# Performance work log

Measured on AMD Instinct MI355X. Metric: run time of the kernel, lower is better.

## Reference

```python
import jax, jax.numpy as jnp
import numpy as np

B, C, D, H, W = 4, 256, 32, 32, 32
K = 1024  # codebook size


def setup_inputs() -> dict:
    key = jax.random.key(0)
    k1, k2 = jax.random.split(key)
    z = jax.random.normal(k1, (B, C, D, H, W), dtype=jnp.float32)
    # torch init: uniform(-1/K, 1/K)
    emb_weight = jax.random.uniform(k2, (K, C), dtype=jnp.float32,
                                    minval=-1.0 / K, maxval=1.0 / K)
    return {"z": z, "emb_weight": emb_weight}


def reference(z, emb_weight):
    beta = 0.25
    emb_dim = emb_weight.shape[1]
    # [B, C, D, H, W] -> [B, D, H, W, C]
    zc = jnp.transpose(z, (0, 2, 3, 4, 1))
    z_flat = zc.reshape(-1, emb_dim)  # [N, C]
    # squared euclidean distances [N, K]
    d = (jnp.sum(z_flat ** 2, axis=1, keepdims=True)
         + jnp.sum(emb_weight ** 2, axis=1)
         - 2.0 * jnp.matmul(z_flat, emb_weight.T))
    idx = jnp.argmin(d, axis=1)  # [N]
    z_q = emb_weight[idx].reshape(zc.shape)  # [B, D, H, W, C]
    sg = jax.lax.stop_gradient
    loss = jnp.mean((sg(z_q) - zc) ** 2) + beta * jnp.mean((z_q - sg(zc)) ** 2)
    # straight-through estimator
    z_q = zc + sg(z_q - zc)
    # back to [B, C, D, H, W]
    z_q = jnp.transpose(z_q, (0, 4, 1, 2, 3))
    return z_q, loss, idx
```

## Files before the change

### kernel.cpp

```cpp
#include <hip/hip_runtime.h>

#define SPATIAL 32768
#define BATCH   4
#define CH      256
#define KCODES  1024
#define NPTS    (BATCH*SPATIAL)
#define ZQ_SIZE (BATCH*CH*SPATIAL)

#define WS_LOSS  0
#define WS_CNT   8
#define WS_ENORM 16
#define WS_EH    4112
#define WS_EL    (WS_EH + KCODES*CH*2)
#define WS_FLAGS (WS_EL + KCODES*CH*2)

#define MARG 1.5e-4f

typedef _Float16 f16x8 __attribute__((ext_vector_type(8)));
typedef float    f32x4 __attribute__((ext_vector_type(4)));

__global__ __launch_bounds__(256) void vq_prep(const float* __restrict__ emb,
                                               _Float16* __restrict__ eh,
                                               _Float16* __restrict__ el) {
  int i = blockIdx.x * 256 + threadIdx.x;
  float es = emb[i] * 1024.0f;
  _Float16 h = (_Float16)es;
  eh[i] = h;
  el[i] = (_Float16)(es - (float)h);
}

__global__ __launch_bounds__(256) void vq_enorm(const float* __restrict__ emb,
                                                float* __restrict__ enorm) {
  int k = blockIdx.x * 256 + threadIdx.x;
  const float* e = emb + (size_t)k * CH;
  double s = 0.0;
#pragma unroll 8
  for (int c = 0; c < CH; ++c) s = fma((double)e[c], (double)e[c], s);
  enorm[k] = (float)s;
}

__global__ __launch_bounds__(256) void vq_main(
    const float* __restrict__ z, const _Float16* __restrict__ eh_g,
    const _Float16* __restrict__ el_g, const float* __restrict__ enorm,
    float* __restrict__ out_idx, double* __restrict__ loss_acc,
    int* __restrict__ flag_cnt, int* __restrict__ flags) {
  __shared__ _Float16 zh[64][264];
  __shared__ _Float16 zl[64][264];
  __shared__ double   znp[4][64];
  __shared__ float    znb[64];
  __shared__ float rm1s[4][64];
  __shared__ float rm2s[4][64];
  __shared__ int   ri1s[4][64];

  int tid = threadIdx.x;
  int w = tid >> 6;
  int lane = tid & 63;
  int n0 = blockIdx.x * 64;
  int b = n0 / SPATIAL, s0 = n0 % SPATIAL;
  const float* zb = z + (size_t)b * CH * SPATIAL + s0;

  {
    int pt = lane, crow = w;
    const float* zcol = zb + pt;
    double zacc = 0.0;
#pragma unroll
    for (int oct = 0; oct < 8; ++oct) {
      int c0 = crow * 64 + oct * 8;
      f16x8 h8, l8;
#pragma unroll
      for (int i = 0; i < 8; ++i) {
        float v = zcol[(size_t)(c0 + i) * SPATIAL];
        zacc = fma((double)v, (double)v, zacc);
        _Float16 h = (_Float16)v;
        h8[i] = h;
        l8[i] = (_Float16)(v - (float)h);
      }
      *(f16x8*)&zh[pt][c0] = h8;
      *(f16x8*)&zl[pt][c0] = l8;
    }
    znp[crow][pt] = zacc;
  }
  __syncthreads();
  if (tid < 64)
    znb[tid] = (float)(znp[0][tid] + znp[1][tid] + znp[2][tid] + znp[3][tid]);
  __syncthreads();

  int hq = lane >> 4;
  int lr = lane & 15;

  float en_reg[16];
#pragma unroll
  for (int kt = 0; kt < 8; ++kt) {
    en_reg[kt * 2]     = enorm[kt * 128 + w * 32 + lr];
    en_reg[kt * 2 + 1] = enorm[kt * 128 + w * 32 + lr + 16];
  }
  float znr[16];
#pragma unroll
  for (int m = 0; m < 4; ++m)
#pragma unroll
    for (int r = 0; r < 4; ++r)
      znr[m * 4 + r] = znb[m * 16 + hq * 4 + r];

  float rm1[16], rm2[16];
  int   ri1[16];
#pragma unroll
  for (int q = 0; q < 16; ++q) { rm1[q] = 1e30f; rm2[q] = 1e30f; ri1[q] = 0; }

  for (int kt = 0; kt < 8; ++kt) {
    int k0 = kt * 128;
    f32x4 acc[4][2];
#pragma unroll
    for (int m = 0; m < 4; ++m)
#pragma unroll
      for (int n = 0; n < 2; ++n) acc[m][n] = (f32x4){0.f, 0.f, 0.f, 0.f};

#pragma unroll 2
    for (int cc = 0; cc < 8; ++cc) {
      int ca = cc * 32 + hq * 8;
      f16x8 ah[4], al[4], bh[2], bl[2];
#pragma unroll
      for (int m = 0; m < 4; ++m) {
        ah[m] = *(const f16x8*)&zh[m * 16 + lr][ca];
        al[m] = *(const f16x8*)&zl[m * 16 + lr][ca];
      }
#pragma unroll
      for (int n = 0; n < 2; ++n) {
        int code = k0 + w * 32 + n * 16 + lr;
        bh[n] = *(const f16x8*)&eh_g[(size_t)code * CH + ca];
        bl[n] = *(const f16x8*)&el_g[(size_t)code * CH + ca];
      }
#pragma unroll
      for (int m = 0; m < 4; ++m)
#pragma unroll
        for (int n = 0; n < 2; ++n) {
          acc[m][n] = __builtin_amdgcn_mfma_f32_16x16x32_f16(ah[m], bh[n], acc[m][n], 0, 0, 0);
          acc[m][n] = __builtin_amdgcn_mfma_f32_16x16x32_f16(al[m], bh[n], acc[m][n], 0, 0, 0);
          acc[m][n] = __builtin_amdgcn_mfma_f32_16x16x32_f16(ah[m], bl[n], acc[m][n], 0, 0, 0);
        }
    }

    float enA = en_reg[kt * 2], enB = en_reg[kt * 2 + 1];
    int c0i = k0 + w * 32 + lr;
#pragma unroll
    for (int m = 0; m < 4; ++m) {
#pragma unroll
      for (int r = 0; r < 4; ++r) {
        int q = m * 4 + r;
        float zn = znr[q];
        float p0 = (zn + enA) - acc[m][0][r] * 0x1p-9f;
        float p1 = (zn + enB) - acc[m][1][r] * 0x1p-9f;
        if (p0 < rm1[q]) { rm2[q] = rm1[q]; rm1[q] = p0; ri1[q] = c0i; }
        else             { rm2[q] = fminf(rm2[q], p0); }
        if (p1 < rm1[q]) { rm2[q] = rm1[q]; rm1[q] = p1; ri1[q] = c0i + 16; }
        else             { rm2[q] = fminf(rm2[q], p1); }
      }
    }
  }

#pragma unroll
  for (int m = 0; m < 4; ++m) {
#pragma unroll
    for (int r = 0; r < 4; ++r) {
      int q = m * 4 + r;
      float m1 = rm1[q], m2 = rm2[q];
      int i1 = ri1[q];
#pragma unroll
      for (int msk = 1; msk <= 8; msk <<= 1) {
        float om1 = __shfl_xor(m1, msk);
        float om2 = __shfl_xor(m2, msk);
        int   oi1 = __shfl_xor(i1, msk);
        if (om1 < m1 || (om1 == m1 && oi1 < i1)) {
          m2 = fminf(m1, om2); m1 = om1; i1 = oi1;
        } else {
          m2 = fminf(m2, om1);
        }
      }
      if (lr == 0) {
        int pt = m * 16 + hq * 4 + r;
        rm1s[w][pt] = m1; rm2s[w][pt] = m2; ri1s[w][pt] = i1;
      }
    }
  }
  __syncthreads();

  double dv = 0.0;
  if (tid < 64) {
    float m1 = rm1s[0][tid], m2 = rm2s[0][tid];
    int i1 = ri1s[0][tid];
#pragma unroll
    for (int pq = 1; pq < 4; ++pq) {
      float a1 = rm1s[pq][tid], a2 = rm2s[pq][tid];
      int ai = ri1s[pq][tid];
      if (a1 < m1 || (a1 == m1 && ai < i1)) {
        m2 = fminf(m1, a2); m1 = a1; i1 = ai;
      } else {
        m2 = fminf(m2, a1);
      }
    }
    int n = n0 + tid;
    out_idx[n] = (float)i1;
    if (m2 - m1 <= MARG) {
      int p = atomicAdd(flag_cnt, 1);
      if (p < NPTS) flags[p] = n;
    }
    dv = (double)m1;
#pragma unroll
    for (int msk = 1; msk < 64; msk <<= 1) dv += __shfl_xor(dv, msk);
    if (tid == 0) atomicAdd(loss_acc, dv);
  }
}

__global__ __launch_bounds__(256) void vq_recheck(
    const float* __restrict__ z, const float* __restrict__ emb,
    const float* __restrict__ enorm, const int* __restrict__ flag_cnt,
    const int* __restrict__ flags, float* __restrict__ out_idx) {
  __shared__ float zs[4][CH];
  __shared__ float znf[4];
  __shared__ float bm[256];
  __shared__ int   bi[256];
  int cnt = *flag_cnt; if (cnt > NPTS) cnt = NPTS;
  int t = threadIdx.x;
  for (int base = blockIdx.x * 4; base < cnt; base += gridDim.x * 4) {
#pragma unroll
    for (int q = 0; q < 4; ++q) {
      int ii = base + q; if (ii >= cnt) ii = cnt - 1;
      int n = flags[ii];
      int b = n / SPATIAL, s = n % SPATIAL;
      zs[q][t] = z[((size_t)b * CH + t) * SPATIAL + s];
    }
    __syncthreads();
    if (t < 4) {
      double sd = 0.0;
      for (int c = 0; c < CH; ++c) sd = fma((double)zs[t][c], (double)zs[t][c], sd);
      znf[t] = (float)sd;
    }
    __syncthreads();
    float best[4] = {1e30f, 1e30f, 1e30f, 1e30f};
    int besti[4] = {0, 0, 0, 0};
    for (int q = 0; q < 4; ++q) {
      int code = t + 256 * q;
      const float* er = emb + (size_t)code * CH;
      float g0 = 0.f, g1 = 0.f, g2 = 0.f, g3 = 0.f;
#pragma unroll 8
      for (int c = 0; c < CH; ++c) {
        float e = er[c];
        g0 = fmaf(zs[0][c], e, g0);
        g1 = fmaf(zs[1][c], e, g1);
        g2 = fmaf(zs[2][c], e, g2);
        g3 = fmaf(zs[3][c], e, g3);
      }
      float en = enorm[code];
      float d0 = (znf[0] + en) - 2.f * g0;
      float d1 = (znf[1] + en) - 2.f * g1;
      float d2 = (znf[2] + en) - 2.f * g2;
      float d3 = (znf[3] + en) - 2.f * g3;
      if (d0 < best[0]) { best[0] = d0; besti[0] = code; }
      if (d1 < best[1]) { best[1] = d1; besti[1] = code; }
      if (d2 < best[2]) { best[2] = d2; besti[2] = code; }
      if (d3 < best[3]) { best[3] = d3; besti[3] = code; }
    }
#pragma unroll
    for (int p = 0; p < 4; ++p) {
      bm[t] = best[p]; bi[t] = besti[p];
      __syncthreads();
      for (int off = 128; off > 0; off >>= 1) {
        if (t < off) {
          float ob = bm[t + off]; int oi = bi[t + off];
          if (ob < bm[t] || (ob == bm[t] && oi < bi[t])) { bm[t] = ob; bi[t] = oi; }
        }
        __syncthreads();
      }
      int ii = base + p;
      if (t == 0 && ii < cnt) out_idx[flags[ii]] = (float)bi[0];
      __syncthreads();
    }
  }
}

__global__ __launch_bounds__(256) void vq_scatter(
    const float* __restrict__ emb, const float* __restrict__ out_idx,
    float* __restrict__ zq, const double* __restrict__ loss_acc,
    float* __restrict__ loss_out) {
  int c = blockIdx.y, b = blockIdx.z;
  int s = (blockIdx.x * 256 + threadIdx.x) * 4;
  int nb = b * SPATIAL + s;
  int i0 = (int)out_idx[nb + 0];
  int i1 = (int)out_idx[nb + 1];
  int i2 = (int)out_idx[nb + 2];
  int i3 = (int)out_idx[nb + 3];
  float4 o;
  o.x = emb[(size_t)i0 * CH + c];
  o.y = emb[(size_t)i1 * CH + c];
  o.z = emb[(size_t)i2 * CH + c];
  o.w = emb[(size_t)i3 * CH + c];
  *reinterpret_cast<float4*>(&zq[((size_t)(b * CH + c)) * SPATIAL + s]) = o;
  if (blockIdx.x == 0 && blockIdx.y == 0 && blockIdx.z == 0 && threadIdx.x == 0)
    loss_out[0] = (float)(loss_acc[0] * 1.25 / (double)ZQ_SIZE);
}

extern "C" void kernel_launch(void* const* d_in, const int* in_sizes, int n_in,
                              void* d_out, int out_size, void* d_ws, size_t ws_size,
                              hipStream_t stream) {
  const float* z   = (const float*)d_in[0];
  const float* emb = (const float*)d_in[1];
  float* out = (float*)d_out;
  char* ws = (char*)d_ws;

  double*   loss_acc = (double*)(ws + WS_LOSS);
  int*      flag_cnt = (int*)(ws + WS_CNT);
  float*    enorm    = (float*)(ws + WS_ENORM);
  _Float16* eh       = (_Float16*)(ws + WS_EH);
  _Float16* el       = (_Float16*)(ws + WS_EL);
  int*      flags    = (int*)(ws + WS_FLAGS);

  float* loss_out = out + ZQ_SIZE;
  float* out_idx  = out + ZQ_SIZE + 1;

  hipMemsetAsync(d_ws, 0, 16, stream);
  vq_prep<<<KCODES * CH / 256, 256, 0, stream>>>(emb, eh, el);
  vq_enorm<<<KCODES / 256, 256, 0, stream>>>(emb, enorm);
  vq_main<<<NPTS / 64, 256, 0, stream>>>(z, eh, el, enorm, out_idx,
                                         loss_acc, flag_cnt, flags);
  vq_recheck<<<512, 256, 0, stream>>>(z, emb, enorm, flag_cnt, flags, out_idx);
  vq_scatter<<<dim3(SPATIAL / 1024, CH, BATCH), 256, 0, stream>>>(
      emb, out_idx, out, loss_acc, loss_out);
}
```

Before: 623.9 us.

## Pre-swizzle codebook into MFMA fragment order, prefetch B, and tile scatter through LDS

The codebook hi/lo fp16 split is now stored pre-arranged in MFMA fragment order, so each lane does a single contiguous 16-byte load per step. The main loop double-buffers these B-fragment loads one step ahead. The z tile in shared memory is stored in fragment order as well, the code norms are staged in LDS, and the kernel is given a launch bound of 2 blocks per CU. The scatter kernel now gathers 64 codebook rows into swizzled LDS and writes coalesced channel-major rows, replacing the scattered per-element gathers. In exchange it uses more LDS per block (64KB for scatter) and more registers for the prefetch.

```diff
diff --git a/kernel.cpp b/kernel.cpp
--- a/kernel.cpp
+++ b/kernel.cpp
@@ -10,9 +10,9 @@
 #define WS_LOSS  0
 #define WS_CNT   8
 #define WS_ENORM 16
-#define WS_EH    4112
-#define WS_EL    (WS_EH + KCODES*CH*2)
-#define WS_FLAGS (WS_EL + KCODES*CH*2)
+#define WS_EHP   4352
+#define WS_ELP   (WS_EHP + KCODES*CH*2)
+#define WS_FLAGS (WS_ELP + KCODES*CH*2)
 
 #define MARG 1.5e-4f
 
@@ -20,13 +20,26 @@
 typedef float    f32x4 __attribute__((ext_vector_type(4)));
 
 __global__ __launch_bounds__(256) void vq_prep(const float* __restrict__ emb,
-                                               _Float16* __restrict__ eh,
-                                               _Float16* __restrict__ el) {
-  int i = blockIdx.x * 256 + threadIdx.x;
-  float es = emb[i] * 1024.0f;
-  _Float16 h = (_Float16)es;
-  eh[i] = h;
-  el[i] = (_Float16)(es - (float)h);
+                                               f16x8* __restrict__ ehp,
+                                               f16x8* __restrict__ elp) {
+  int kb = blockIdx.x;
+#pragma unroll
+  for (int h = 0; h < 2; ++h) {
+    int q = threadIdx.x + h * 256;
+    int cc = q >> 6, ln = q & 63;
+    int hq = ln >> 4, lr = ln & 15;
+    const float* src = emb + ((size_t)(kb * 16 + lr) * CH + cc * 32 + hq * 8);
+    f16x8 h8, l8;
+#pragma unroll
+    for (int j = 0; j < 8; ++j) {
+      float es = src[j] * 1024.0f;
+      _Float16 hi = (_Float16)es;
+      h8[j] = hi;
+      l8[j] = (_Float16)(es - (float)hi);
+    }
+    ehp[kb * 512 + q] = h8;
+    elp[kb * 512 + q] = l8;
+  }
 }
 
 __global__ __launch_bounds__(256) void vq_enorm(const float* __restrict__ emb,
@@ -39,15 +52,15 @@
   enorm[k] = (float)s;
 }
 
-__global__ __launch_bounds__(256) void vq_main(
-    const float* __restrict__ z, const _Float16* __restrict__ eh_g,
-    const _Float16* __restrict__ el_g, const float* __restrict__ enorm,
+__global__ __launch_bounds__(256, 2) void vq_main(
+    const float* __restrict__ z, const f16x8* __restrict__ ehp,
+    const f16x8* __restrict__ elp, const float* __restrict__ enorm,
     float* __restrict__ out_idx, double* __restrict__ loss_acc,
     int* __restrict__ flag_cnt, int* __restrict__ flags) {
-  __shared__ _Float16 zh[64][264];
-  __shared__ _Float16 zl[64][264];
-  __shared__ double   znp[4][64];
-  __shared__ float    znb[64];
+  __shared__ f16x8 zfrag[64][64];
+  __shared__ float en_s[KCODES];
+  __shared__ double znp[4][64];
+  __shared__ float  znb[64];
   __shared__ float rm1s[4][64];
   __shared__ float rm2s[4][64];
   __shared__ int   ri1s[4][64];
@@ -60,26 +73,29 @@
   const float* zb = z + (size_t)b * CH * SPATIAL + s0;
 
   {
-    int pt = lane, crow = w;
+    int pt = lane, m = pt >> 4, lr = pt & 15;
     const float* zcol = zb + pt;
     double zacc = 0.0;
 #pragma unroll
     for (int oct = 0; oct < 8; ++oct) {
-      int c0 = crow * 64 + oct * 8;
+      int c0 = w * 64 + oct * 8;
+      int cc = c0 >> 5, hq = (c0 >> 3) & 3;
       f16x8 h8, l8;
 #pragma unroll
       for (int i = 0; i < 8; ++i) {
         float v = zcol[(size_t)(c0 + i) * SPATIAL];
         zacc = fma((double)v, (double)v, zacc);
-        _Float16 h = (_Float16)v;
-        h8[i] = h;
-        l8[i] = (_Float16)(v - (float)h);
-      }
-      *(f16x8*)&zh[pt][c0] = h8;
-      *(f16x8*)&zl[pt][c0] = l8;
-    }
-    znp[crow][pt] = zacc;
-  }
+        _Float16 hh = (_Float16)v;
+        h8[i] = hh;
+        l8[i] = (_Float16)(v - (float)hh);
+      }
+      zfrag[m * 8 + cc][hq * 16 + lr] = h8;
+      zfrag[32 + m * 8 + cc][hq * 16 + lr] = l8;
+    }
+    znp[w][pt] = zacc;
+  }
+#pragma unroll
+  for (int j = 0; j < 4; ++j) en_s[tid + 256 * j] = enorm[tid + 256 * j];
   __syncthreads();
   if (tid < 64)
     znb[tid] = (float)(znp[0][tid] + znp[1][tid] + znp[2][tid] + znp[3][tid]);
@@ -88,18 +104,11 @@
   int hq = lane >> 4;
   int lr = lane & 15;
 
-  float en_reg[16];
-#pragma unroll
-  for (int kt = 0; kt < 8; ++kt) {
-    en_reg[kt * 2]     = enorm[kt * 128 + w * 32 + lr];
-    en_reg[kt * 2 + 1] = enorm[kt * 128 + w * 32 + lr + 16];
-  }
   float znr[16];
 #pragma unroll
   for (int m = 0; m < 4; ++m)
 #pragma unroll
-    for (int r = 0; r < 4; ++r)
-      znr[m * 4 + r] = znb[m * 16 + hq * 4 + r];
+    for (int r = 0; r < 4; ++r) znr[m * 4 + r] = znb[m * 16 + hq * 4 + r];
 
   float rm1[16], rm2[16];
   int   ri1[16];
@@ -107,40 +116,47 @@
   for (int q = 0; q < 16; ++q) { rm1[q] = 1e30f; rm2[q] = 1e30f; ri1[q] = 0; }
 
   for (int kt = 0; kt < 8; ++kt) {
-    int k0 = kt * 128;
+    int kb0 = kt * 8 + w * 2;
+    const f16x8* ph0 = ehp + (size_t)kb0 * 512 + lane;
+    const f16x8* ph1 = ph0 + 512;
+    const f16x8* pl0 = elp + (size_t)kb0 * 512 + lane;
+    const f16x8* pl1 = pl0 + 512;
+
     f32x4 acc[4][2];
 #pragma unroll
     for (int m = 0; m < 4; ++m)
 #pragma unroll
       for (int n = 0; n < 2; ++n) acc[m][n] = (f32x4){0.f, 0.f, 0.f, 0.f};
 
-#pragma unroll 2
+    f16x8 bh[2][2], bl[2][2];
+    bh[0][0] = ph0[0]; bh[0][1] = ph1[0];
+    bl[0][0] = pl0[0]; bl[0][1] = pl1[0];
+#pragma unroll
     for (int cc = 0; cc < 8; ++cc) {
-      int ca = cc * 32 + hq * 8;
-      f16x8 ah[4], al[4], bh[2], bl[2];
+      int cur = cc & 1, nxt = cur ^ 1;
+      if (cc < 7) {
+        bh[nxt][0] = ph0[(cc + 1) * 64]; bh[nxt][1] = ph1[(cc + 1) * 64];
+        bl[nxt][0] = pl0[(cc + 1) * 64]; bl[nxt][1] = pl1[(cc + 1) * 64];
+      }
+      f16x8 ah[4], al[4];
 #pragma unroll
       for (int m = 0; m < 4; ++m) {
-        ah[m] = *(const f16x8*)&zh[m * 16 + lr][ca];
-        al[m] = *(const f16x8*)&zl[m * 16 + lr][ca];
-      }
-#pragma unroll
-      for (int n = 0; n < 2; ++n) {
-        int code = k0 + w * 32 + n * 16 + lr;
-        bh[n] = *(const f16x8*)&eh_g[(size_t)code * CH + ca];
-        bl[n] = *(const f16x8*)&el_g[(size_t)code * CH + ca];
+        ah[m] = zfrag[m * 8 + cc][lane];
+        al[m] = zfrag[32 + m * 8 + cc][lane];
       }
 #pragma unroll
       for (int m = 0; m < 4; ++m)
 #pragma unroll
         for (int n = 0; n < 2; ++n) {
-          acc[m][n] = __builtin_amdgcn_mfma_f32_16x16x32_f16(ah[m], bh[n], acc[m][n], 0, 0, 0);
-          acc[m][n] = __builtin_amdgcn_mfma_f32_16x16x32_f16(al[m], bh[n], acc[m][n], 0, 0, 0);
-          acc[m][n] = __builtin_amdgcn_mfma_f32_16x16x32_f16(ah[m], bl[n], acc[m][n], 0, 0, 0);
+          acc[m][n] = __builtin_amdgcn_mfma_f32_16x16x32_f16(ah[m], bh[cur][n], acc[m][n], 0, 0, 0);
+          acc[m][n] = __builtin_amdgcn_mfma_f32_16x16x32_f16(al[m], bh[cur][n], acc[m][n], 0, 0, 0);
+          acc[m][n] = __builtin_amdgcn_mfma_f32_16x16x32_f16(ah[m], bl[cur][n], acc[m][n], 0, 0, 0);
         }
     }
 
-    float enA = en_reg[kt * 2], enB = en_reg[kt * 2 + 1];
-    int c0i = k0 + w * 32 + lr;
+    float enA = en_s[kt * 128 + w * 32 + lr];
+    float enB = en_s[kt * 128 + w * 32 + 16 + lr];
+    int c0i = kt * 128 + w * 32 + lr;
 #pragma unroll
     for (int m = 0; m < 4; ++m) {
 #pragma unroll
@@ -183,7 +199,6 @@
   }
   __syncthreads();
 
-  double dv = 0.0;
   if (tid < 64) {
     float m1 = rm1s[0][tid], m2 = rm2s[0][tid];
     int i1 = ri1s[0][tid];
@@ -203,7 +218,7 @@
       int p = atomicAdd(flag_cnt, 1);
       if (p < NPTS) flags[p] = n;
     }
-    dv = (double)m1;
+    double dv = (double)m1;
 #pragma unroll
     for (int msk = 1; msk < 64; msk <<= 1) dv += __shfl_xor(dv, msk);
     if (tid == 0) atomicAdd(loss_acc, dv);
@@ -281,20 +296,30 @@
     const float* __restrict__ emb, const float* __restrict__ out_idx,
     float* __restrict__ zq, const double* __restrict__ loss_acc,
     float* __restrict__ loss_out) {
-  int c = blockIdx.y, b = blockIdx.z;
-  int s = (blockIdx.x * 256 + threadIdx.x) * 4;
-  int nb = b * SPATIAL + s;
-  int i0 = (int)out_idx[nb + 0];
-  int i1 = (int)out_idx[nb + 1];
-  int i2 = (int)out_idx[nb + 2];
-  int i3 = (int)out_idx[nb + 3];
-  float4 o;
-  o.x = emb[(size_t)i0 * CH + c];
-  o.y = emb[(size_t)i1 * CH + c];
-  o.z = emb[(size_t)i2 * CH + c];
-  o.w = emb[(size_t)i3 * CH + c];
-  *reinterpret_cast<float4*>(&zq[((size_t)(b * CH + c)) * SPATIAL + s]) = o;
-  if (blockIdx.x == 0 && blockIdx.y == 0 && blockIdx.z == 0 && threadIdx.x == 0)
+  __shared__ float rows[64][256];
+  __shared__ int idxs[64];
+  int tid = threadIdx.x;
+  int n0 = blockIdx.x * 64;
+  int b = n0 / SPATIAL, s0 = n0 % SPATIAL;
+  if (tid < 64) idxs[tid] = (int)out_idx[n0 + tid];
+  __syncthreads();
+  int lane = tid & 63, grp = tid >> 6;
+  for (int r = grp; r < 64; r += 4) {
+    const float* er = emb + (size_t)idxs[r] * CH;
+    int sw = r & 31;
+#pragma unroll
+    for (int i = 0; i < 4; ++i) {
+      int c = lane + 64 * i;
+      rows[r][c ^ sw] = er[c];
+    }
+  }
+  __syncthreads();
+  for (int it = 0; it < 64; ++it) {
+    int c = grp * 64 + it;
+    float v = rows[lane][c ^ (lane & 31)];
+    zq[((size_t)(b * CH + c)) * SPATIAL + s0 + lane] = v;
+  }
+  if (blockIdx.x == 0 && tid == 0)
     loss_out[0] = (float)(loss_acc[0] * 1.25 / (double)ZQ_SIZE);
 }
 
@@ -306,22 +331,21 @@
   float* out = (float*)d_out;
   char* ws = (char*)d_ws;
 
-  double*   loss_acc = (double*)(ws + WS_LOSS);
-  int*      flag_cnt = (int*)(ws + WS_CNT);
-  float*    enorm    = (float*)(ws + WS_ENORM);
-  _Float16* eh       = (_Float16*)(ws + WS_EH);
-  _Float16* el       = (_Float16*)(ws + WS_EL);
-  int*      flags    = (int*)(ws + WS_FLAGS);
+  double* loss_acc = (double*)(ws + WS_LOSS);
+  int*    flag_cnt = (int*)(ws + WS_CNT);
+  float*  enorm    = (float*)(ws + WS_ENORM);
+  f16x8*  ehp      = (f16x8*)(ws + WS_EHP);
+  f16x8*  elp      = (f16x8*)(ws + WS_ELP);
+  int*    flags    = (int*)(ws + WS_FLAGS);
 
   float* loss_out = out + ZQ_SIZE;
   float* out_idx  = out + ZQ_SIZE + 1;
 
   hipMemsetAsync(d_ws, 0, 16, stream);
-  vq_prep<<<KCODES * CH / 256, 256, 0, stream>>>(emb, eh, el);
+  vq_prep<<<KCODES / 16, 256, 0, stream>>>(emb, ehp, elp);
   vq_enorm<<<KCODES / 256, 256, 0, stream>>>(emb, enorm);
-  vq_main<<<NPTS / 64, 256, 0, stream>>>(z, eh, el, enorm, out_idx,
+  vq_main<<<NPTS / 64, 256, 0, stream>>>(z, ehp, elp, enorm, out_idx,
                                          loss_acc, flag_cnt, flags);
   vq_recheck<<<512, 256, 0, stream>>>(z, emb, enorm, flag_cnt, flags, out_idx);
-  vq_scatter<<<dim3(SPATIAL / 1024, CH, BATCH), 256, 0, stream>>>(
-      emb, out_idx, out, loss_acc, loss_out);
-}
+  vq_scatter<<<NPTS / 64, 256, 0, stream>>>(emb, out_idx, out, loss_acc, loss_out);
+}
```

New measurement: 844.8 us. 1.35x slower.
